# Performance work log

Measured on AMD Instinct MI355X. Metric: run time of the kernel, lower is better.

The kernel has to match this reference:

```python
import jax, jax.numpy as jnp
import numpy as np

N, E, D, H = 50000, 800000, 128, 8
HD = D // H
EPS = 1e-5


def _layernorm(x, w, b):
    # Custom LayerNorm from the repo: divides by (unbiased std + eps), not sqrt(var+eps)
    mu = x.mean(axis=-1, keepdims=True)
    sd = x.std(axis=-1, keepdims=True, ddof=1)
    return (x - mu) / (sd + EPS) * w + b


def setup_inputs() -> dict:
    key = jax.random.key(0)
    ks = jax.random.split(key, 16)
    s = 1.0 / np.sqrt(D)
    inp = {
        "feats": jax.random.normal(ks[0], (N, D), jnp.float32),
        "edge_index": jax.random.randint(ks[1], (E, 2), 0, N, jnp.int32),
        "Wq": jax.random.normal(ks[2], (D, D), jnp.float32) * s,
        "bq": jnp.zeros((D,), jnp.float32),
        "Wk": jax.random.normal(ks[3], (D, D), jnp.float32) * s,
        "bk": jnp.zeros((D,), jnp.float32),
        "Wv": jax.random.normal(ks[4], (D, D), jnp.float32) * s,
        "bv": jnp.zeros((D,), jnp.float32),
        "Wo": jax.random.normal(ks[5], (D, D), jnp.float32) * s,
        "bo": jnp.zeros((D,), jnp.float32),
        "ln1_w": jnp.ones((D,), jnp.float32),
        "ln1_b": jnp.zeros((D,), jnp.float32),
        "ln2_w": jnp.ones((D,), jnp.float32),
        "ln2_b": jnp.zeros((D,), jnp.float32),
        "W1": jax.random.normal(ks[6], (4 * D, D), jnp.float32) * s,
        "b1": jnp.zeros((4 * D,), jnp.float32),
        "W2": jax.random.normal(ks[7], (D, 4 * D), jnp.float32) * (1.0 / np.sqrt(4 * D)),
        "b2": jnp.zeros((D,), jnp.float32),
    }
    return inp


def reference(feats, edge_index, Wq, bq, Wk, bk, Wv, bv, Wo, bo,
              ln1_w, ln1_b, ln2_w, ln2_b, W1, b1, W2, b2):
    n = feats.shape[0]
    row, col = edge_index[:, 0], edge_index[:, 1]

    # --- multi-head dot-product attention over edges (dropout = identity, eval mode) ---
    x2 = _layernorm(feats, ln1_w, ln1_b)
    q = (x2 @ Wq.T + bq).reshape(n, H, HD)
    k = (x2 @ Wk.T + bk).reshape(n, H, HD)
    v = (x2 @ Wv.T + bv).reshape(n, H, HD)

    # per-edge scores: q[col] . k[row] / sqrt(head_dim)  -> [E, H]
    scores = jnp.einsum('ehd,ehd->eh', q[col], k[row]) / np.sqrt(HD).astype(np.float32)

    # scatter softmax normalized over groups of `row`
    smax = jax.ops.segment_max(scores, row, num_segments=n)       # [N, H]
    ex = jnp.exp(scores - smax[row])                              # [E, H]
    denom = jax.ops.segment_sum(ex, row, num_segments=n)         # [N, H]
    alpha = ex / denom[row]                                       # [E, H]

    # weighted messages, aggregated at col via scatter_add
    msg = alpha[:, :, None] * v[row]                              # [E, H, HD]
    agg = jax.ops.segment_sum(msg, col, num_segments=n).reshape(n, D)
    att = agg @ Wo.T + bo

    feats = feats + att  # residual 1

    # --- MLP block: note ReLU after BOTH linears (fc_dims=[4D, D], D != 1) ---
    x2 = _layernorm(feats, ln2_w, ln2_b)
    h = jax.nn.relu(x2 @ W1.T + b1)
    h = jax.nn.relu(h @ W2.T + b2)
    feats = feats + h  # residual 2
    return feats
```

## Files before the change

kernel.cpp:

```cpp
#include <hip/hip_runtime.h>
#include <hip/hip_bf16.h>
#include <math.h>

#define H_HEADS 8
constexpr float LN_EPS = 1e-5f;
constexpr int NBCH = 64;
constexpr int NSEG = 4;

using short8 = __attribute__((ext_vector_type(8))) short;
using f32x4  = __attribute__((ext_vector_type(4))) float;
using f32x2  = __attribute__((ext_vector_type(2))) float;
using half2v = __attribute__((ext_vector_type(2))) _Float16;

#if defined(__has_builtin)
#  if __has_builtin(__builtin_amdgcn_fdot2)
#    define HAS_FDOT2 1
#  endif
#  if __has_builtin(__builtin_amdgcn_cvt_pk_f32_fp8) && __has_builtin(__builtin_amdgcn_cvt_pk_fp8_f32)
#    define HAS_CVT_FP8 1
#  endif
#endif
#ifndef HAS_FDOT2
#  define HAS_FDOT2 0
#endif
#ifndef HAS_CVT_FP8
#  define HAS_CVT_FP8 0
#endif

__device__ __forceinline__ ushort f2bf(float v){
  __hip_bfloat16 h = __float2bfloat16(v);
  return *reinterpret_cast<ushort*>(&h);
}
__device__ __forceinline__ float bf2f(ushort u){
  return __uint_as_float(((unsigned)u) << 16);
}

__device__ __forceinline__ unsigned char f32_to_fp8(float v){
#if HAS_CVT_FP8
  return (unsigned char)(__builtin_amdgcn_cvt_pk_fp8_f32(v, v, 0, false) & 0xff);
#else
  _Float16 hv = (_Float16)v;
  ushort h = __builtin_bit_cast(ushort, hv);
  unsigned sign = (h >> 8) & 0x80;
  unsigned p = h & 0x7fff;
  if (p < 0x2400u) return (unsigned char)sign;
  unsigned q = (p - 0x2000u + 0x40u) >> 7;
  if (q > 0x7eu) q = 0x7eu;
  return (unsigned char)(sign | q);
#endif
}
__device__ __forceinline__ float fp8_to_f32(unsigned b){
  unsigned p = b & 0x7f;
  ushort hbits = (ushort)(((b & 0x80) << 8) | (p ? ((p << 7) + 0x2000u) : 0));
  _Float16 hv = __builtin_bit_cast(_Float16, hbits);
  return (float)hv;
}

__device__ __forceinline__ void stage16(const ushort* g, ushort* l){
  __builtin_amdgcn_global_load_lds((const __attribute__((address_space(1))) unsigned*)g,
                                   (__attribute__((address_space(3))) unsigned*)l,
                                   16, 0, 0);
}

__global__ void ln_kernel(const float* __restrict__ x, const float* __restrict__ w,
                          const float* __restrict__ b, ushort* __restrict__ out, int nrows){
  int wid = threadIdx.x >> 6, lane = threadIdx.x & 63;
  int r = blockIdx.x * (blockDim.x >> 6) + wid;
  if (r >= nrows) return;
  float2 v = ((const float2*)(x + (size_t)r*128))[lane];
  float s = v.x + v.y;
  #pragma unroll
  for (int o = 32; o; o >>= 1) s += __shfl_xor(s, o);
  float mu = s * (1.0f/128.0f);
  float d0 = v.x - mu, d1 = v.y - mu;
  float ss = d0*d0 + d1*d1;
  #pragma unroll
  for (int o = 32; o; o >>= 1) ss += __shfl_xor(ss, o);
  float sd = sqrtf(ss * (1.0f/127.0f));
  float inv = 1.0f / (sd + LN_EPS);
  float2 wv = ((const float2*)w)[lane];
  float2 bv = ((const float2*)b)[lane];
  ushort2 o2 = { f2bf(d0*inv*wv.x + bv.x), f2bf(d1*inv*wv.y + bv.y) };
  ((ushort2*)(out + (size_t)r*128))[lane] = o2;
}

struct CvtArgs { const float* s[6]; ushort* d[6]; int cnt[6]; };
__global__ void cvt6_kernel(CvtArgs a){
  int w = blockIdx.y;
  int i = blockIdx.x*blockDim.x + threadIdx.x;
  if (i < a.cnt[w]) a.d[w][i] = f2bf(a.s[w][i]);
}

template<int K, int RELU, int RESID, int OUTMODE>
__device__ __forceinline__ void gemm_lds_body(
    const ushort* __restrict__ A, const ushort* __restrict__ W,
    const float* __restrict__ bias, const float* __restrict__ resid,
    void* __restrict__ out, int M, int Nout, int cb, ushort* Wl){
  constexpr int NCH = K / 128;
  int t = threadIdx.x;
  int wid = t >> 6, lane = t & 63;
  int mb = blockIdx.x * 128 + wid * 16;
  int lrow = lane & 15, kgrp = lane >> 4;
  int row = mb + lrow;
  bool waveok = mb < M;
  bool rowok = row < M;
  const ushort* arow = A + (size_t)(rowok ? row : (M-1)) * K + kgrp*8;

  f32x4 acc[8] = {};
  short8 af[2][4];

  #pragma unroll
  for (int p = 0; p < 4; ++p){
    int L = p*512 + t;
    int colp = L >> 4, sp = L & 15;
    stage16(W + (size_t)colp*K + ((sp ^ (colp & 7)) << 3),
            (ushort*)((char*)Wl + ((size_t)(p*512 + (t & ~63)))*16));
  }
  if (waveok){
    #pragma unroll
    for (int kk = 0; kk < 4; ++kk)
      af[0][kk] = *(const short8*)(arow + kk*32);
  }

  #pragma unroll
  for (int ci = 0; ci < NCH; ++ci){
    __syncthreads();
    int cur = ci & 1;
    if (waveok){
      if (ci + 1 < NCH){
        #pragma unroll
        for (int kk = 0; kk < 4; ++kk)
          af[cur^1][kk] = *(const short8*)(arow + (ci+1)*128 + kk*32);
      }
      #pragma unroll
      for (int kk = 0; kk < 4; ++kk){
        #pragma unroll
        for (int nt = 0; nt < 8; ++nt){
          int colc = nt*16 + lrow;
          int g = kk*4 + kgrp;
          short8 bfv = *(const short8*)((const char*)Wl + colc*256 + ((g ^ (colc & 7))*16));
          acc[nt] = __builtin_amdgcn_mfma_f32_16x16x32_bf16(af[cur][kk], bfv, acc[nt], 0, 0, 0);
        }
      }
    }
    if (ci + 1 < NCH){
      __syncthreads();
      const ushort* Wc = W + (ci+1)*128;
      #pragma unroll
      for (int p = 0; p < 4; ++p){
        int L = p*512 + t;
        int colp = L >> 4, sp = L & 15;
        stage16(Wc + (size_t)colp*K + ((sp ^ (colp & 7)) << 3),
                (ushort*)((char*)Wl + ((size_t)(p*512 + (t & ~63)))*16));
      }
    }
  }
  if (!waveok) return;

  int r0 = mb + kgrp*4;
  #pragma unroll
  for (int nt = 0; nt < 8; ++nt){
    int c = cb + nt*16 + lrow;
    float bsum = bias[c];
    #pragma unroll
    for (int i = 0; i < 4; ++i){
      int r = r0 + i;
      if (r >= M) continue;
      float v = acc[nt][i] + bsum;
      if (RELU)  v = fmaxf(v, 0.0f);
      if (RESID) v += resid[(size_t)r*Nout + c];
      if (OUTMODE == 1) ((ushort*)out)[(size_t)r*Nout + c] = f2bf(v);
      else if (OUTMODE == 2){
        _Float16 hv = (_Float16)v;
        ((ushort*)out)[(size_t)r*Nout + c] = __builtin_bit_cast(ushort, hv);
      } else ((float*)out)[(size_t)r*Nout + c] = v;
    }
  }
}

template<int K, int RELU, int RESID, int OUTMODE>
__global__ __launch_bounds__(512) void gemm_lds(
    const ushort* __restrict__ A, const ushort* __restrict__ Wfull,
    const float* __restrict__ bias, const float* __restrict__ resid,
    void* __restrict__ out, int M, int Nout){
  __shared__ __align__(16) ushort Wl[16384];
  int cb = blockIdx.y * 128;
  gemm_lds_body<K,RELU,RESID,OUTMODE>(A, Wfull + (size_t)cb*K, bias, resid, out, M, Nout, cb, Wl);
}

__global__ __launch_bounds__(512) void qkv_fused(
    const ushort* __restrict__ A, const ushort* __restrict__ Wcat,
    const float* __restrict__ bq, const float* __restrict__ bk, const float* __restrict__ bv,
    unsigned char* __restrict__ qb8, ushort* __restrict__ kb, ushort* __restrict__ vb, int M){
  constexpr int K = 128;
  __shared__ __align__(16) ushort Wl[16384];
  int t = threadIdx.x;
  int wid = t >> 6, lane = t & 63;
  int mb = blockIdx.x * 128 + wid * 16;
  int lrow = lane & 15, kgrp = lane >> 4;
  int row = mb + lrow;
  bool waveok = mb < M;
  bool rowok = row < M;
  const ushort* arow = A + (size_t)(rowok ? row : (M-1)) * K + kgrp*8;

  short8 af[4];
  if (waveok){
    #pragma unroll
    for (int kk = 0; kk < 4; ++kk)
      af[kk] = *(const short8*)(arow + kk*32);
  }

  #pragma unroll
  for (int y = 0; y < 3; ++y){
    if (y) __syncthreads();
    const ushort* W = Wcat + (size_t)y*16384;
    #pragma unroll
    for (int p = 0; p < 4; ++p){
      int L = p*512 + t;
      int colp = L >> 4, sp = L & 15;
      stage16(W + (size_t)colp*K + ((sp ^ (colp & 7)) << 3),
              (ushort*)((char*)Wl + ((size_t)(p*512 + (t & ~63)))*16));
    }
    __syncthreads();
    if (waveok){
      const float* bias = (y==0) ? bq : (y==1) ? bk : bv;
      f32x4 acc[8] = {};
      #pragma unroll
      for (int kk = 0; kk < 4; ++kk){
        #pragma unroll
        for (int nt = 0; nt < 8; ++nt){
          int colc = nt*16 + lrow;
          int g = kk*4 + kgrp;
          short8 bfv = *(const short8*)((const char*)Wl + colc*256 + ((g ^ (colc & 7))*16));
          acc[nt] = __builtin_amdgcn_mfma_f32_16x16x32_bf16(af[kk], bfv, acc[nt], 0, 0, 0);
        }
      }
      int r0 = mb + kgrp*4;
      #pragma unroll
      for (int nt = 0; nt < 8; ++nt){
        int c = nt*16 + lrow;
        float bsum = bias[c];
        #pragma unroll
        for (int i = 0; i < 4; ++i){
          int r = r0 + i;
          if (r >= M) continue;
          float v = acc[nt][i] + bsum;
          if (y == 0)      qb8[(size_t)r*128 + c] = f32_to_fp8(v);
          else if (y == 1){
            _Float16 hv = (_Float16)v;
            kb[(size_t)r*128 + c] = __builtin_bit_cast(ushort, hv);
          } else           vb[(size_t)r*128 + c] = f2bf(v);
        }
      }
    }
  }
}

__global__ __launch_bounds__(512) void gemm_wo_ln2(
    const ushort* __restrict__ A, const ushort* __restrict__ W,
    const float* __restrict__ bias, const float* __restrict__ feats,
    const float* __restrict__ lnw, const float* __restrict__ lnb,
    float* __restrict__ outp, ushort* __restrict__ x2b, int M){
  constexpr int K = 128;
  __shared__ __align__(16) ushort Wl[16384];
  int t = threadIdx.x;
  int wid = t >> 6, lane = t & 63;
  int mb = blockIdx.x * 128 + wid * 16;
  int lrow = lane & 15, kgrp = lane >> 4;
  int row = mb + lrow;
  bool waveok = mb < M;
  bool rowok = row < M;
  const ushort* arow = A + (size_t)(rowok ? row : (M-1)) * K + kgrp*8;

  f32x4 acc[8] = {};
  short8 af[4];

  #pragma unroll
  for (int p = 0; p < 4; ++p){
    int L = p*512 + t;
    int colp = L >> 4, sp = L & 15;
    stage16(W + (size_t)colp*K + ((sp ^ (colp & 7)) << 3),
            (ushort*)((char*)Wl + ((size_t)(p*512 + (t & ~63)))*16));
  }
  if (waveok){
    #pragma unroll
    for (int kk = 0; kk < 4; ++kk)
      af[kk] = *(const short8*)(arow + kk*32);
  }
  __syncthreads();
  if (!waveok) return;

  #pragma unroll
  for (int kk = 0; kk < 4; ++kk){
    #pragma unroll
    for (int nt = 0; nt < 8; ++nt){
      int colc = nt*16 + lrow;
      int g = kk*4 + kgrp;
      short8 bfv = *(const short8*)((const char*)Wl + colc*256 + ((g ^ (colc & 7))*16));
      acc[nt] = __builtin_amdgcn_mfma_f32_16x16x32_bf16(af[kk], bfv, acc[nt], 0, 0, 0);
    }
  }

  int r0 = mb + kgrp*4;
  float vv[8][4];
  float lw[8], lb[8];
  #pragma unroll
  for (int nt = 0; nt < 8; ++nt){
    int c = nt*16 + lrow;
    float bsum = bias[c];
    lw[nt] = lnw[c]; lb[nt] = lnb[c];
    #pragma unroll
    for (int i = 0; i < 4; ++i){
      int r = r0 + i;
      float v = 0.f;
      if (r < M){
        v = acc[nt][i] + bsum + feats[(size_t)r*128 + c];
        outp[(size_t)r*128 + c] = v;
      }
      vv[nt][i] = v;
    }
  }
  #pragma unroll
  for (int i = 0; i < 4; ++i){
    int r = r0 + i;
    float s = 0.f;
    #pragma unroll
    for (int nt = 0; nt < 8; ++nt) s += vv[nt][i];
    #pragma unroll
    for (int o = 1; o < 16; o <<= 1) s += __shfl_xor(s, o);
    float mu = s * (1.0f/128.0f);
    float ss = 0.f;
    float d[8];
    #pragma unroll
    for (int nt = 0; nt < 8; ++nt){ d[nt] = vv[nt][i] - mu; ss += d[nt]*d[nt]; }
    #pragma unroll
    for (int o = 1; o < 16; o <<= 1) ss += __shfl_xor(ss, o);
    float sd = sqrtf(ss * (1.0f/127.0f));
    float inv = 1.0f / (sd + LN_EPS);
    if (r < M){
      #pragma unroll
      for (int nt = 0; nt < 8; ++nt){
        int c = nt*16 + lrow;
        x2b[(size_t)r*128 + c] = f2bf(d[nt]*inv*lw[nt] + lb[nt]);
      }
    }
  }
}

__global__ __launch_bounds__(256) void hist_seg2(const int* __restrict__ ei,
    unsigned* __restrict__ copies, int E, int n, int nw, int chunk, int nsb){
  __shared__ unsigned hh[12544];
  int b = blockIdx.x, s = blockIdx.y, t = threadIdx.x;
  int bin0 = s * nsb;
  int bin1 = min(bin0 + nsb, n);
  int words = (bin1 - bin0 + 1) >> 1;
  for (int i = t; i < 2*words; i += 256) hh[i] = 0;
  __syncthreads();
  int lo = b*chunk, hi = min(lo + chunk, E);
  for (int e = lo + t; e < hi; e += 256){
    int2 rc = ((const int2*)ei)[e];
    if (rc.x >= bin0 && rc.x < bin1)
      atomicAdd(&hh[(rc.x - bin0) >> 1], 1u << ((rc.x & 1)*16));
    if (rc.y >= bin0 && rc.y < bin1)
      atomicAdd(&hh[words + ((rc.y - bin0) >> 1)], 1u << ((rc.y & 1)*16));
  }
  __syncthreads();
  unsigned* d0 = copies + (size_t)b*nw + (bin0 >> 1);
  unsigned* d1 = copies + (size_t)(NBCH + b)*nw + (bin0 >> 1);
  for (int i = t; i < words; i += 256){ d0[i] = hh[i]; d1[i] = hh[words + i]; }
}

__global__ __launch_bounds__(256) void scan_fold(const unsigned* __restrict__ copies,
    int* __restrict__ cnt2, ushort* __restrict__ choff, int n, int nw){
  int y = blockIdx.y;
  int bin = blockIdx.x*256 + threadIdx.x;
  if (bin >= n) return;
  const unsigned* cp = copies + (size_t)y*NBCH*nw + (bin >> 1);
  int sh = (bin & 1)*16;
  int run = 0;
  for (int b = 0; b < NBCH; ++b){
    int c = (int)((cp[(size_t)b*nw] >> sh) & 0xffffu);
    choff[((size_t)y*NBCH + b)*n + bin] = (ushort)run;
    run += c;
  }
  cnt2[(size_t)y*n + bin] = run;
}

__global__ __launch_bounds__(256) void scan_reduce(const int* __restrict__ cnt0,
                                                   int* __restrict__ partial, int n, int nb){
  const int* cnt = cnt0 + (size_t)blockIdx.y * n;
  int t = threadIdx.x;
  int base = blockIdx.x*1024 + t*4;
  int s = 0;
  #pragma unroll
  for (int j = 0; j < 4; ++j){ int i = base+j; if (i < n) s += cnt[i]; }
  __shared__ int sm[256];
  sm[t] = s; __syncthreads();
  for (int off = 128; off; off >>= 1){
    if (t < off) sm[t] += sm[t+off];
    __syncthreads();
  }
  if (t == 0) partial[blockIdx.y*nb + blockIdx.x] = sm[0];
}

__global__ __launch_bounds__(256) void scan_mid(int* __restrict__ partial, int nb,
                                                int* __restrict__ rptr, int* __restrict__ cptr, int n){
  int y = blockIdx.y;
  int* p = partial + y*nb;
  int t = threadIdx.x;
  __shared__ int sm[256];
  sm[t] = (t < nb) ? p[t] : 0;
  __syncthreads();
  for (int off = 1; off < 256; off <<= 1){
    int v = (t >= off) ? sm[t-off] : 0;
    __syncthreads();
    sm[t] += v;
    __syncthreads();
  }
  if (t < nb) p[t] = (t == 0) ? 0 : sm[t-1];
  if (t == 0) (y ? cptr : rptr)[n] = sm[255];
}

__global__ __launch_bounds__(256) void scan_scatter(const int* __restrict__ cnt0,
                                                    const int* __restrict__ partial,
                                                    int* __restrict__ rptr, int* __restrict__ cptr,
                                                    int n, int nb){
  int y = blockIdx.y;
  const int* cnt = cnt0 + (size_t)y * n;
  int* ptr = y ? cptr : rptr;
  int t = threadIdx.x;
  int base = blockIdx.x*1024 + t*4;
  int v[4]; int s = 0;
  #pragma unroll
  for (int j = 0; j < 4; ++j){ int i = base+j; v[j] = (i<n)?cnt[i]:0; s += v[j]; }
  __shared__ int sm[256];
  sm[t] = s; __syncthreads();
  for (int off = 1; off < 256; off <<= 1){
    int x = (t >= off) ? sm[t-off] : 0;
    __syncthreads();
    sm[t] += x;
    __syncthreads();
  }
  int pre = partial[y*nb + blockIdx.x] + ((t==0)?0:sm[t-1]);
  #pragma unroll
  for (int j = 0; j < 4; ++j){
    int i = base+j;
    if (i < n){ ptr[i] = pre; pre += v[j]; }
  }
}

__global__ __launch_bounds__(256) void fill_r_seg(const int* __restrict__ ei,
    const int* __restrict__ rptr, const ushort* __restrict__ choffR,
    int* __restrict__ rcol, int* __restrict__ pose, int E, int n, int chunk, int nsb){
  __shared__ unsigned hh[8192];
  int b = blockIdx.x, s = blockIdx.y, t = threadIdx.x;
  int bin0 = s * nsb;
  int bin1 = min(bin0 + nsb, n);
  int words = (bin1 - bin0 + 1) >> 1;
  for (int i = t; i < words; i += 256) hh[i] = 0;
  __syncthreads();
  const ushort* chb = choffR + (size_t)b*n;
  int lo = b*chunk, hi = min(lo + chunk, E);
  for (int e = lo + t; e < hi; e += 256){
    int2 rc = ((const int2*)ei)[e];
    int bin = rc.x;
    if (bin < bin0 || bin >= bin1) continue;
    int sh = (bin & 1)*16;
    unsigned old = atomicAdd(&hh[(bin - bin0) >> 1], 1u << sh);
    int rank = (int)((old >> sh) & 0xffffu);
    int pos = rptr[bin] + (int)chb[bin] + rank;
    rcol[pos] = rc.y;
    pose[e] = pos;
  }
}

__global__ __launch_bounds__(256) void fill_c_seg(const int* __restrict__ ei,
    const int* __restrict__ cptr, const ushort* __restrict__ choffC,
    const int* __restrict__ pose, int* __restrict__ crow, int* __restrict__ cposr,
    int E, int n, int chunk, int nsb){
  __shared__ unsigned hh[8192];
  int b = blockIdx.x, s = blockIdx.y, t = threadIdx.x;
  int bin0 = s * nsb;
  int bin1 = min(bin0 + nsb, n);
  int words = (bin1 - bin0 + 1) >> 1;
  for (int i = t; i < words; i += 256) hh[i] = 0;
  __syncthreads();
  const ushort* chb = choffC + (size_t)b*n;
  int lo = b*chunk, hi = min(lo + chunk, E);
  for (int e = lo + t; e < hi; e += 256){
    int2 rc = ((const int2*)ei)[e];
    int bin = rc.y;
    if (bin < bin0 || bin >= bin1) continue;
    int sh = (bin & 1)*16;
    unsigned old = atomicAdd(&hh[(bin - bin0) >> 1], 1u << sh);
    int rank = (int)((old >> sh) & 0xffffu);
    int pos = cptr[bin] + (int)chb[bin] + rank;
    crow[pos] = rc.x;
    cposr[pose[e]] = pos;
  }
}

__device__ __forceinline__ float qdot16q8(const unsigned char* __restrict__ qb8, int c, int h,
                                          const float* kf){
  const uint4* qp = (const uint4*)(qb8 + (size_t)c*128 + h*16);
  uint4 q = *qp;
  unsigned w[4] = {q.x, q.y, q.z, q.w};
  float s = 0.f;
  #pragma unroll
  for (int i = 0; i < 4; ++i){
#if HAS_CVT_FP8
    f32x2 lo = __builtin_amdgcn_cvt_pk_f32_fp8(w[i], false);
    f32x2 hi = __builtin_amdgcn_cvt_pk_f32_fp8(w[i], true);
    s = fmaf(lo[0], kf[4*i+0], s);
    s = fmaf(lo[1], kf[4*i+1], s);
    s = fmaf(hi[0], kf[4*i+2], s);
    s = fmaf(hi[1], kf[4*i+3], s);
#else
    #pragma unroll
    for (int j = 0; j < 4; ++j)
      s = fmaf(fp8_to_f32((w[i] >> (8*j)) & 0xffu), kf[4*i+j], s);
#endif
  }
  return s * 0.25f;
}

template<int NS>
__device__ __forceinline__ void softmax_rows(const unsigned char* __restrict__ qb8,
    const int* __restrict__ rcol, const int* __restrict__ cposr,
    ushort* __restrict__ cbuf, const float* kf, int lo, int hi, int h, int el,
    int rl, int cpl){
  float sreg[NS];
  float m = -1e30f;
  #pragma unroll
  for (int ts = 0; ts < NS; ++ts){
    int c = __shfl(rl, el + ts*8);
    int j = lo + el + ts*8;
    float s = -1e30f;
    if (j < hi) s = qdot16q8(qb8, c, h, kf);
    sreg[ts] = s;
    m = fmaxf(m, s);
  }
  if (NS == 8)
    for (int j = lo + el + 64; j < hi; j += 8)
      m = fmaxf(m, qdot16q8(qb8, rcol[j], h, kf));
  #pragma unroll
  for (int o = 8; o < 64; o <<= 1) m = fmaxf(m, __shfl_xor(m, o));

  float d = 0.f;
  #pragma unroll
  for (int ts = 0; ts < NS; ++ts){
    int j = lo + el + ts*8;
    if (j < hi){ float e = __expf(sreg[ts] - m); sreg[ts] = e; d += e; }
  }
  if (NS == 8)
    for (int j = lo + el + 64; j < hi; j += 8)
      d += __expf(qdot16q8(qb8, rcol[j], h, kf) - m);
  #pragma unroll
  for (int o = 8; o < 64; o <<= 1) d += __shfl_xor(d, o);
  float invd = 1.0f / d;

  #pragma unroll
  for (int ts = 0; ts < NS; ++ts){
    int cp = __shfl(cpl, el + ts*8);
    int j = lo + el + ts*8;
    if (j < hi) cbuf[(size_t)cp*8 + h] = f2bf(sreg[ts] * invd);
  }
  if (NS == 8)
    for (int j = lo + el + 64; j < hi; j += 8){
      float s = qdot16q8(qb8, rcol[j], h, kf);
      cbuf[(size_t)cposr[j]*8 + h] = f2bf(__expf(s - m) * invd);
    }
}

__global__ void row_softmax_kernel(const unsigned char* __restrict__ qb8,
                                   const ushort* __restrict__ kb,
                                   const int* __restrict__ rptr, const int* __restrict__ rcol,
                                   const int* __restrict__ cposr,
                                   ushort* __restrict__ cbuf, int n){
  int wid = threadIdx.x >> 6, lane = threadIdx.x & 63;
  int r = blockIdx.x * (blockDim.x >> 6) + wid;
  if (r >= n) return;
  int lo = rptr[r], hi = rptr[r+1];
  if (lo >= hi) return;
  int h = lane & 7, el = lane >> 3;

  int jl = lo + lane;
  bool jok = jl < hi;
  int rl  = rcol [jok ? jl : lo];
  int cpl = cposr[jok ? jl : lo];

  float kf[16];
  {
    const int4* kp = (const int4*)(kb + (size_t)r*128 + h*16);
    int4 k0 = kp[0], k1 = kp[1];
    int kw[8] = {k0.x,k0.y,k0.z,k0.w,k1.x,k1.y,k1.z,k1.w};
    #pragma unroll
    for (int i = 0; i < 8; ++i){
      half2v k2 = __builtin_bit_cast(half2v, kw[i]);
      kf[2*i]   = (float)k2.x;
      kf[2*i+1] = (float)k2.y;
    }
  }

  int deg = hi - lo;
  if (deg <= 16)      softmax_rows<2>(qb8, rcol, cposr, cbuf, kf, lo, hi, h, el, rl, cpl);
  else if (deg <= 32) softmax_rows<4>(qb8, rcol, cposr, cbuf, kf, lo, hi, h, el, rl, cpl);
  else                softmax_rows<8>(qb8, rcol, cposr, cbuf, kf, lo, hi, h, el, rl, cpl);
}

__global__ void agg_kernel(const ushort* __restrict__ vb, const ushort* __restrict__ cbuf,
                           const int* __restrict__ cptr, const int* __restrict__ crow,
                           ushort* __restrict__ aggb, int n){
  int wid = threadIdx.x >> 6, lane = threadIdx.x & 63;
  int node = blockIdx.x * (blockDim.x >> 6) + wid;
  if (node >= n) return;
  int lo = cptr[node], hi = cptr[node+1];
  int deg = hi - lo;
  int oct = lane >> 3, l8 = lane & 7;

  int jl = lo + lane;
  int crl = crow[jl < hi ? jl : lo];

  float acc[16] = {};
  int tmax = (deg + 7) >> 3;
  for (int ts = 0; ts < tmax; ++ts){
    int li = oct + ts*8;
    int row = __shfl(crl, li & 63);
    if (li < deg){
      if (li >= 64) row = crow[lo + li];
      float a = bf2f(cbuf[(size_t)(lo + li)*8 + l8]);
      const short8* vp = (const short8*)(vb + (size_t)row*128 + l8*16);
      short8 v0 = vp[0], v1 = vp[1];
      #pragma unroll
      for (int i = 0; i < 8; ++i){
        acc[i]   = fmaf(a, bf2f((ushort)v0[i]), acc[i]);
        acc[8+i] = fmaf(a, bf2f((ushort)v1[i]), acc[8+i]);
      }
    }
  }
  #pragma unroll
  for (int i = 0; i < 16; ++i){
    acc[i] += __shfl_xor(acc[i], 8);
    acc[i] += __shfl_xor(acc[i], 16);
    acc[i] += __shfl_xor(acc[i], 32);
  }
  if (oct == 0){
    short8 o0, o1;
    #pragma unroll
    for (int i = 0; i < 8; ++i){ o0[i] = (short)f2bf(acc[i]); o1[i] = (short)f2bf(acc[8+i]); }
    short8* op = (short8*)(aggb + (size_t)node*128 + l8*16);
    op[0] = o0; op[1] = o1;
  }
}

extern "C" void kernel_launch(void* const* d_in, const int* in_sizes, int n_in,
                              void* d_out, int out_size, void* d_ws, size_t ws_size,
                              hipStream_t stream){
  const float* feats = (const float*)d_in[0];
  const int*   ei    = (const int*)  d_in[1];
  const float* Wq = (const float*)d_in[2];
  const float* bq = (const float*)d_in[3];
  const float* Wk = (const float*)d_in[4];
  const float* bk = (const float*)d_in[5];
  const float* Wv = (const float*)d_in[6];
  const float* bv = (const float*)d_in[7];
  const float* Wo = (const float*)d_in[8];
  const float* bo = (const float*)d_in[9];
  const float* ln1w = (const float*)d_in[10];
  const float* ln1b = (const float*)d_in[11];
  const float* ln2w = (const float*)d_in[12];
  const float* ln2b = (const float*)d_in[13];
  const float* W1 = (const float*)d_in[14];
  const float* b1 = (const float*)d_in[15];
  const float* W2 = (const float*)d_in[16];
  const float* b2 = (const float*)d_in[17];
  float* outp = (float*)d_out;

  int n = in_sizes[0] / 128;
  int E = in_sizes[1] / 2;
  int nw = (n + 1) >> 1;
  int chunk = (E + NBCH - 1) / NBCH;
  int nsb = (((n + NSEG - 1) / NSEG) + 1) & ~1;

  const size_t ND  = (size_t)n * 128;
  const size_t ND2 = ND / 2;
  const size_t EH  = (size_t)E * H_HEADS;

  float* ws = (float*)d_ws;
  ushort* x2b  = (ushort*)ws;
  unsigned char* qb8 = (unsigned char*)(ws + ND2);
  ushort* kb   = (ushort*)(ws + 2*ND2);
  ushort* vb   = (ushort*)(ws + 3*ND2);
  ushort* cbuf = (ushort*)(ws + 4*ND2);
  ushort* aggb = (ushort*)(ws + 4*ND2 + EH/2);
  int* crow    = (int*)(ws + 5*ND2 + EH/2);
  int* cposr   = crow + E;
  int* rcol    = cposr + E;
  int* pose    = rcol + E;
  int* rptr    = pose + E;
  int* cptr    = rptr + (n + 4);
  int* cnt2    = cptr + (n + 4);
  ushort* choff = (ushort*)(cnt2 + 2*n);
  unsigned* copies = (unsigned*)(choff + (size_t)2*NBCH*n);
  int* partial = (int*)(copies + (size_t)2*NBCH*nw);
  ushort* wbuf = (ushort*)(partial + 512);
  ushort* Wqb = wbuf;
  ushort* Wkb = Wqb + 16384;
  ushort* Wvb = Wkb + 16384;
  ushort* Wob = Wvb + 16384;
  ushort* W1b = Wob + 16384;
  ushort* W2b = W1b + 65536;
  ushort* h1  = (ushort*)qb8;

  CvtArgs ca;
  ca.s[0]=Wq; ca.s[1]=Wk; ca.s[2]=Wv; ca.s[3]=Wo; ca.s[4]=W1; ca.s[5]=W2;
  ca.d[0]=Wqb; ca.d[1]=Wkb; ca.d[2]=Wvb; ca.d[3]=Wob; ca.d[4]=W1b; ca.d[5]=W2b;
  ca.cnt[0]=ca.cnt[1]=ca.cnt[2]=ca.cnt[3]=16384; ca.cnt[4]=ca.cnt[5]=65536;
  cvt6_kernel<<<dim3(65536/256, 6), 256, 0, stream>>>(ca);

  int nb = (n + 1023)/1024;
  hist_seg2 <<<dim3(NBCH,NSEG), 256, 0, stream>>>(ei, copies, E, n, nw, chunk, nsb);
  scan_fold <<<dim3((n+255)/256,2), 256, 0, stream>>>(copies, cnt2, choff, n, nw);
  scan_reduce <<<dim3(nb,2), 256, 0, stream>>>(cnt2, partial, n, nb);
  scan_mid    <<<dim3(1,2),  256, 0, stream>>>(partial, nb, rptr, cptr, n);
  scan_scatter<<<dim3(nb,2), 256, 0, stream>>>(cnt2, partial, rptr, cptr, n, nb);
  fill_r_seg<<<dim3(NBCH,NSEG), 256, 0, stream>>>(ei, rptr, choff,                  rcol, pose, E, n, chunk, nsb);
  fill_c_seg<<<dim3(NBCH,NSEG), 256, 0, stream>>>(ei, cptr, choff + (size_t)NBCH*n, pose, crow, cposr, E, n, chunk, nsb);

  ln_kernel<<<(n+3)/4, 256, 0, stream>>>(feats, ln1w, ln1b, x2b, n);

  int gm = (n + 127)/128;
  qkv_fused<<<gm, 512, 0, stream>>>(x2b, Wqb, bq, bk, bv, qb8, kb, vb, n);

  row_softmax_kernel<<<(n+3)/4, 256, 0, stream>>>(qb8, kb, rptr, rcol, cposr, cbuf, n);

  agg_kernel<<<(n+3)/4, 256, 0, stream>>>(vb, cbuf, cptr, crow, aggb, n);

  gemm_wo_ln2<<<gm, 512, 0, stream>>>(aggb, Wob, bo, feats, ln2w, ln2b, outp, x2b, n);

  gemm_lds<128,1,0,1><<<dim3(gm,4), 512, 0, stream>>>(x2b, W1b, b1, nullptr, h1,  n, 512);
  gemm_lds<512,1,1,0><<<dim3(gm,1), 512, 0, stream>>>(h1,  W2b, b2, outp,    outp, n, 128);
}
```

Baseline: 274.6 us.

## Fuse LayerNorm1 into QKV GEMM and merge scan fold/reduce kernels

Removes the standalone ln_kernel. The QKV kernel now reads fp32 feats directly and computes per-row mean and unbiased std with cross-lane shuffles, writing bf16 A fragments in registers. This avoids one bf16 intermediate write and read plus a launch. The scan pipeline also folds the block reduction into scan_fold and uses 256-bin partials, which drops scan_reduce. In exchange the QKV kernel uses more registers (32 floats per thread), and scan_mid now has more partials to process.

Result: faster. 265.9 us, median of 2 (-3.2%).

```diff
diff --git a/kernel.cpp b/kernel.cpp
--- a/kernel.cpp
+++ b/kernel.cpp
@@ -13,15 +13,9 @@
 using half2v = __attribute__((ext_vector_type(2))) _Float16;
 
 #if defined(__has_builtin)
-#  if __has_builtin(__builtin_amdgcn_fdot2)
-#    define HAS_FDOT2 1
-#  endif
 #  if __has_builtin(__builtin_amdgcn_cvt_pk_f32_fp8) && __has_builtin(__builtin_amdgcn_cvt_pk_fp8_f32)
 #    define HAS_CVT_FP8 1
 #  endif
-#endif
-#ifndef HAS_FDOT2
-#  define HAS_FDOT2 0
 #endif
 #ifndef HAS_CVT_FP8
 #  define HAS_CVT_FP8 0
@@ -60,28 +54,6 @@
   __builtin_amdgcn_global_load_lds((const __attribute__((address_space(1))) unsigned*)g,
                                    (__attribute__((address_space(3))) unsigned*)l,
                                    16, 0, 0);
-}
-
-__global__ void ln_kernel(const float* __restrict__ x, const float* __restrict__ w,
-                          const float* __restrict__ b, ushort* __restrict__ out, int nrows){
-  int wid = threadIdx.x >> 6, lane = threadIdx.x & 63;
-  int r = blockIdx.x * (blockDim.x >> 6) + wid;
-  if (r >= nrows) return;
-  float2 v = ((const float2*)(x + (size_t)r*128))[lane];
-  float s = v.x + v.y;
-  #pragma unroll
-  for (int o = 32; o; o >>= 1) s += __shfl_xor(s, o);
-  float mu = s * (1.0f/128.0f);
-  float d0 = v.x - mu, d1 = v.y - mu;
-  float ss = d0*d0 + d1*d1;
-  #pragma unroll
-  for (int o = 32; o; o >>= 1) ss += __shfl_xor(ss, o);
-  float sd = sqrtf(ss * (1.0f/127.0f));
-  float inv = 1.0f / (sd + LN_EPS);
-  float2 wv = ((const float2*)w)[lane];
-  float2 bv = ((const float2*)b)[lane];
-  ushort2 o2 = { f2bf(d0*inv*wv.x + bv.x), f2bf(d1*inv*wv.y + bv.y) };
-  ((ushort2*)(out + (size_t)r*128))[lane] = o2;
 }
 
 struct CvtArgs { const float* s[6]; ushort* d[6]; int cnt[6]; };
@@ -189,7 +161,8 @@
 }
 
 __global__ __launch_bounds__(512) void qkv_fused(
-    const ushort* __restrict__ A, const ushort* __restrict__ Wcat,
+    const float* __restrict__ feats, const ushort* __restrict__ Wcat,
+    const float* __restrict__ ln1w, const float* __restrict__ ln1b,
     const float* __restrict__ bq, const float* __restrict__ bk, const float* __restrict__ bv,
     unsigned char* __restrict__ qb8, ushort* __restrict__ kb, ushort* __restrict__ vb, int M){
   constexpr int K = 128;
@@ -201,13 +174,40 @@
   int row = mb + lrow;
   bool waveok = mb < M;
   bool rowok = row < M;
-  const ushort* arow = A + (size_t)(rowok ? row : (M-1)) * K + kgrp*8;
+  int rclamp = rowok ? row : (M-1);
+  const float* frow = feats + (size_t)rclamp*K + kgrp*8;
+
+  float fx[32];
+  #pragma unroll
+  for (int kk = 0; kk < 4; ++kk){
+    float4 a = *(const float4*)(frow + kk*32);
+    float4 b = *(const float4*)(frow + kk*32 + 4);
+    fx[kk*8+0]=a.x; fx[kk*8+1]=a.y; fx[kk*8+2]=a.z; fx[kk*8+3]=a.w;
+    fx[kk*8+4]=b.x; fx[kk*8+5]=b.y; fx[kk*8+6]=b.z; fx[kk*8+7]=b.w;
+  }
+  float s = 0.f;
+  #pragma unroll
+  for (int i = 0; i < 32; ++i) s += fx[i];
+  s += __shfl_xor(s, 16); s += __shfl_xor(s, 32);
+  float mu = s * (1.0f/128.0f);
+  float ss = 0.f;
+  #pragma unroll
+  for (int i = 0; i < 32; ++i){ fx[i] -= mu; ss += fx[i]*fx[i]; }
+  ss += __shfl_xor(ss, 16); ss += __shfl_xor(ss, 32);
+  float inv = 1.0f / (sqrtf(ss * (1.0f/127.0f)) + LN_EPS);
 
   short8 af[4];
-  if (waveok){
-    #pragma unroll
-    for (int kk = 0; kk < 4; ++kk)
-      af[kk] = *(const short8*)(arow + kk*32);
+  #pragma unroll
+  for (int kk = 0; kk < 4; ++kk){
+    const float* wp = ln1w + kgrp*8 + kk*32;
+    const float* bp = ln1b + kgrp*8 + kk*32;
+    float4 w0 = *(const float4*)wp,  w1 = *(const float4*)(wp+4);
+    float4 b0 = *(const float4*)bp,  b1 = *(const float4*)(bp+4);
+    float wv[8] = {w0.x,w0.y,w0.z,w0.w,w1.x,w1.y,w1.z,w1.w};
+    float bvv[8]= {b0.x,b0.y,b0.z,b0.w,b1.x,b1.y,b1.z,b1.w};
+    #pragma unroll
+    for (int j = 0; j < 8; ++j)
+      af[kk][j] = (short)f2bf(fx[kk*8+j]*inv*wv[j] + bvv[j]);
   }
 
   #pragma unroll
@@ -370,37 +370,31 @@
   for (int i = t; i < words; i += 256){ d0[i] = hh[i]; d1[i] = hh[words + i]; }
 }
 
-__global__ __launch_bounds__(256) void scan_fold(const unsigned* __restrict__ copies,
-    int* __restrict__ cnt2, ushort* __restrict__ choff, int n, int nw){
+__global__ __launch_bounds__(256) void scan_fold2(const unsigned* __restrict__ copies,
+    int* __restrict__ cnt2, ushort* __restrict__ choff, int* __restrict__ partial,
+    int n, int nw, int npb){
   int y = blockIdx.y;
-  int bin = blockIdx.x*256 + threadIdx.x;
-  if (bin >= n) return;
-  const unsigned* cp = copies + (size_t)y*NBCH*nw + (bin >> 1);
-  int sh = (bin & 1)*16;
+  int t = threadIdx.x;
+  int bin = blockIdx.x*256 + t;
   int run = 0;
-  for (int b = 0; b < NBCH; ++b){
-    int c = (int)((cp[(size_t)b*nw] >> sh) & 0xffffu);
-    choff[((size_t)y*NBCH + b)*n + bin] = (ushort)run;
-    run += c;
-  }
-  cnt2[(size_t)y*n + bin] = run;
-}
-
-__global__ __launch_bounds__(256) void scan_reduce(const int* __restrict__ cnt0,
-                                                   int* __restrict__ partial, int n, int nb){
-  const int* cnt = cnt0 + (size_t)blockIdx.y * n;
-  int t = threadIdx.x;
-  int base = blockIdx.x*1024 + t*4;
-  int s = 0;
-  #pragma unroll
-  for (int j = 0; j < 4; ++j){ int i = base+j; if (i < n) s += cnt[i]; }
+  if (bin < n){
+    const unsigned* cp = copies + (size_t)y*NBCH*nw + (bin >> 1);
+    int sh = (bin & 1)*16;
+    for (int b = 0; b < NBCH; ++b){
+      int c = (int)((cp[(size_t)b*nw] >> sh) & 0xffffu);
+      choff[((size_t)y*NBCH + b)*n + bin] = (ushort)run;
+      run += c;
+    }
+    cnt2[(size_t)y*n + bin] = run;
+  }
   __shared__ int sm[256];
-  sm[t] = s; __syncthreads();
+  sm[t] = (bin < n) ? run : 0;
+  __syncthreads();
   for (int off = 128; off; off >>= 1){
     if (t < off) sm[t] += sm[t+off];
     __syncthreads();
   }
-  if (t == 0) partial[blockIdx.y*nb + blockIdx.x] = sm[0];
+  if (t == 0) partial[y*npb + blockIdx.x] = sm[0];
 }
 
 __global__ __launch_bounds__(256) void scan_mid(int* __restrict__ partial, int nb,
@@ -421,32 +415,24 @@
   if (t == 0) (y ? cptr : rptr)[n] = sm[255];
 }
 
-__global__ __launch_bounds__(256) void scan_scatter(const int* __restrict__ cnt0,
-                                                    const int* __restrict__ partial,
-                                                    int* __restrict__ rptr, int* __restrict__ cptr,
-                                                    int n, int nb){
+__global__ __launch_bounds__(256) void scan_scatter2(const int* __restrict__ cnt2,
+    const int* __restrict__ partial, int* __restrict__ rptr, int* __restrict__ cptr,
+    int n, int npb){
   int y = blockIdx.y;
-  const int* cnt = cnt0 + (size_t)y * n;
   int* ptr = y ? cptr : rptr;
   int t = threadIdx.x;
-  int base = blockIdx.x*1024 + t*4;
-  int v[4]; int s = 0;
-  #pragma unroll
-  for (int j = 0; j < 4; ++j){ int i = base+j; v[j] = (i<n)?cnt[i]:0; s += v[j]; }
+  int bin = blockIdx.x*256 + t;
+  int v = (bin < n) ? cnt2[(size_t)y*n + bin] : 0;
   __shared__ int sm[256];
-  sm[t] = s; __syncthreads();
+  sm[t] = v;
+  __syncthreads();
   for (int off = 1; off < 256; off <<= 1){
     int x = (t >= off) ? sm[t-off] : 0;
     __syncthreads();
     sm[t] += x;
     __syncthreads();
   }
-  int pre = partial[y*nb + blockIdx.x] + ((t==0)?0:sm[t-1]);
-  #pragma unroll
-  for (int j = 0; j < 4; ++j){
-    int i = base+j;
-    if (i < n){ ptr[i] = pre; pre += v[j]; }
-  }
+  if (bin < n) ptr[bin] = partial[y*npb + blockIdx.x] + sm[t] - v;
 }
 
 __global__ __launch_bounds__(256) void fill_r_seg(const int* __restrict__ ei,
@@ -681,6 +667,7 @@
   int nw = (n + 1) >> 1;
   int chunk = (E + NBCH - 1) / NBCH;
   int nsb = (((n + NSEG - 1) / NSEG) + 1) & ~1;
+  int npb = (n + 255) / 256;
 
   const size_t ND  = (size_t)n * 128;
   const size_t ND2 = ND / 2;
@@ -718,19 +705,15 @@
   ca.cnt[0]=ca.cnt[1]=ca.cnt[2]=ca.cnt[3]=16384; ca.cnt[4]=ca.cnt[5]=65536;
   cvt6_kernel<<<dim3(65536/256, 6), 256, 0, stream>>>(ca);
 
-  int nb = (n + 1023)/1024;
-  hist_seg2 <<<dim3(NBCH,NSEG), 256, 0, stream>>>(ei, copies, E, n, nw, chunk, nsb);
-  scan_fold <<<dim3((n+255)/256,2), 256, 0, stream>>>(copies, cnt2, choff, n, nw);
-  scan_reduce <<<dim3(nb,2), 256, 0, stream>>>(cnt2, partial, n, nb);
-  scan_mid    <<<dim3(1,2),  256, 0, stream>>>(partial, nb, rptr, cptr, n);
-  scan_scatter<<<dim3(nb,2), 256, 0, stream>>>(cnt2, partial, rptr, cptr, n, nb);
+  hist_seg2   <<<dim3(NBCH,NSEG), 256, 0, stream>>>(ei, copies, E, n, nw, chunk, nsb);
+  scan_fold2  <<<dim3(npb,2), 256, 0, stream>>>(copies, cnt2, choff, partial, n, nw, npb);
+  scan_mid    <<<dim3(1,2),   256, 0, stream>>>(partial, npb, rptr, cptr, n);
+  scan_scatter2<<<dim3(npb,2),256, 0, stream>>>(cnt2, partial, rptr, cptr, n, npb);
   fill_r_seg<<<dim3(NBCH,NSEG), 256, 0, stream>>>(ei, rptr, choff,                  rcol, pose, E, n, chunk, nsb);
   fill_c_seg<<<dim3(NBCH,NSEG), 256, 0, stream>>>(ei, cptr, choff + (size_t)NBCH*n, pose, crow, cposr, E, n, chunk, nsb);
 
-  ln_kernel<<<(n+3)/4, 256, 0, stream>>>(feats, ln1w, ln1b, x2b, n);
-
   int gm = (n + 127)/128;
-  qkv_fused<<<gm, 512, 0, stream>>>(x2b, Wqb, bq, bk, bv, qb8, kb, vb, n);
+  qkv_fused<<<gm, 512, 0, stream>>>(feats, Wqb, ln1w, ln1b, bq, bk, bv, qb8, kb, vb, n);
 
   row_softmax_kernel<<<(n+3)/4, 256, 0, stream>>>(qb8, kb, rptr, rcol, cposr, cbuf, n);
 
```
